# Kernel optimization log

Hardware: AMD Instinct MI355X
Metric: run time of the kernel (lower is better)

## Reference

```python
import jax, jax.numpy as jnp
import numpy as np

N = 50000     # nodes
E = 800000    # edges (avg degree 16)
DIN = 128     # in_size
DH = 256      # hidden_size
P = 100000    # pos/neg edge pairs


def _w(key, fan_in, shape):
    return jax.random.normal(key, shape, jnp.float32) * (1.0 / np.sqrt(fan_in))


def setup_inputs() -> dict:
    key = jax.random.key(0)
    ks = jax.random.split(key, 24)
    inp = {}
    inp['x'] = jax.random.normal(ks[0], (N, DIN), jnp.float32)
    inp['edge_src'] = jax.random.randint(ks[1], (E,), 0, N, dtype=jnp.int32)
    inp['edge_dst'] = jax.random.randint(ks[2], (E,), 0, N, dtype=jnp.int32)
    inp['pos_src'] = jax.random.randint(ks[3], (P,), 0, N, dtype=jnp.int32)
    inp['pos_dst'] = jax.random.randint(ks[4], (P,), 0, N, dtype=jnp.int32)
    inp['neg_src'] = jax.random.randint(ks[5], (P,), 0, N, dtype=jnp.int32)
    inp['neg_dst'] = jax.random.randint(ks[6], (P,), 0, N, dtype=jnp.int32)
    # SAGEConv layers: fc_self + fc_neigh + bias
    dims = [(DIN, DH), (DH, DH), (DH, DH)]
    for i, (di, do) in enumerate(dims):
        inp[f'Ws{i}'] = _w(ks[7 + 3 * i], di, (di, do))
        inp[f'Wn{i}'] = _w(ks[8 + 3 * i], di, (di, do))
        inp[f'b{i}'] = jnp.zeros((do,), jnp.float32)
    # predictor MLP: DH -> DH -> DH -> 1
    inp['Wp1'] = _w(ks[16], DH, (DH, DH)); inp['bp1'] = jnp.zeros((DH,), jnp.float32)
    inp['Wp2'] = _w(ks[17], DH, (DH, DH)); inp['bp2'] = jnp.zeros((DH,), jnp.float32)
    inp['Wp3'] = _w(ks[18], DH, (DH, 1)); inp['bp3'] = jnp.zeros((1,), jnp.float32)
    return inp


def _sage_layer(h, src, dst, Ws, Wn, b):
    # mean aggregation over incoming edges, then fc_self(h) + fc_neigh(agg) + b
    n = h.shape[0]
    msg = h[src]                                              # [E, d] gather
    deg = jax.ops.segment_sum(jnp.ones((src.shape[0],), h.dtype), dst, num_segments=n)
    agg = jax.ops.segment_sum(msg, dst, num_segments=n)
    agg = agg / jnp.maximum(deg, 1.0)[:, None]
    return h @ Ws + agg @ Wn + b


def reference(x, edge_src, edge_dst, pos_src, pos_dst, neg_src, neg_dst,
              Ws0, Wn0, b0, Ws1, Wn1, b1, Ws2, Wn2, b2,
              Wp1, bp1, Wp2, bp2, Wp3, bp3):
    h = x
    layers = [(Ws0, Wn0, b0), (Ws1, Wn1, b1), (Ws2, Wn2, b2)]
    for i, (Ws, Wn, bb) in enumerate(layers):
        h = _sage_layer(h, edge_src, edge_dst, Ws, Wn, bb)
        if i < len(layers) - 1:
            h = jax.nn.relu(h)

    def predictor(e):
        z = jax.nn.relu(e @ Wp1 + bp1)
        z = jax.nn.relu(z @ Wp2 + bp2)
        return z @ Wp3 + bp3

    hidden_pos = predictor(h[pos_src] * h[pos_dst])   # [P, 1]
    hidden_neg = predictor(h[neg_src] * h[neg_dst])   # [P, 1]
    return (hidden_pos, hidden_neg)
```

## Files before the change

### kernel.cpp

```cpp
#include <hip/hip_runtime.h>
#include <hip/hip_bf16.h>

#define CDIV(a, b) (((a) + (b) - 1) / (b))

typedef __attribute__((ext_vector_type(8))) __bf16 bf16x8;
typedef __attribute__((ext_vector_type(2))) __bf16 bf16x2;
typedef __attribute__((ext_vector_type(4))) float f32x4;

__device__ __forceinline__ float bf2f(unsigned short u) {
  union { unsigned int i; float f; } c; c.i = ((unsigned int)u) << 16; return c.f;
}
__device__ __forceinline__ unsigned short f2bf(float f) {
  union { float f; unsigned int i; } c; c.f = f;
  unsigned int r = c.i + 0x7fffu + ((c.i >> 16) & 1u);
  return (unsigned short)(r >> 16);
}
__device__ __forceinline__ unsigned int cvt2(float a, float b) {
  bf16x2 v; v[0] = (__bf16)a; v[1] = (__bf16)b;
  union { bf16x2 v; unsigned int u; } c; c.v = v; return c.u;
}
__device__ __forceinline__ unsigned short cvt1(float a) {
  __bf16 b = (__bf16)a;
  union { __bf16 b; unsigned short u; } c; c.b = b; return c.u;
}

__global__ void k_detect(const unsigned short* __restrict__ xq, int nsamp, int* __restrict__ flagp) {
  __shared__ float sm[256];
  int t = threadIdx.x;
  float mx = 0.f;
  for (int i = t; i < nsamp; i += 256) {
    float v = bf2f(xq[i]);
    if (!(v == v)) v = 1e30f;
    mx = fmaxf(mx, fabsf(v));
  }
  sm[t] = mx; __syncthreads();
  for (int o = 128; o > 0; o >>= 1) {
    if (t < o) sm[t] = fmaxf(sm[t], sm[t + o]);
    __syncthreads();
  }
  if (t == 0) *flagp = (sm[0] > 1e6f) ? 1 : 0;
}

__global__ void k_cvt7(const void* p0, const void* p1, const void* p2, const void* p3,
                       const void* p4, const void* p5, const void* p6,
                       float* d0, float* d1, float* d2, float* d3,
                       float* d4, float* d5, float* d6, const int* __restrict__ flagp) {
  int b = blockIdx.x, t = threadIdx.x;
  const void* s = 0; float* d = 0; int n = 256;
  switch (b) {
    case 0: s = p0; d = d0; break;
    case 1: s = p1; d = d1; break;
    case 2: s = p2; d = d2; break;
    case 3: s = p3; d = d3; break;
    case 4: s = p4; d = d4; break;
    case 5: s = p5; d = d5; break;
    default: s = p6; d = d6; n = 1; break;
  }
  if (t < n) d[t] = (*flagp) ? ((const float*)s)[t] : bf2f(((const unsigned short*)s)[t]);
}

__global__ void k_wh(const void* __restrict__ W, unsigned short* __restrict__ Bth,
                     int K, const int* __restrict__ flagp) {
  int i = blockIdx.x * 256 + threadIdx.x;
  if (i >= K * 256) return;
  int k = i >> 8, n = i & 255;
  float v = (*flagp) ? ((const float*)W)[i] : bf2f(((const unsigned short*)W)[i]);
  Bth[(size_t)n * K + k] = f2bf(v);
}

__global__ void k_xbf16(const void* __restrict__ x, unsigned short* __restrict__ Xb, int n,
                        const int* __restrict__ flagp) {
  int i = blockIdx.x * 256 + threadIdx.x;
  if (i >= n) return;
  float v = (*flagp) ? ((const float*)x)[i] : bf2f(((const unsigned short*)x)[i]);
  Xb[i] = f2bf(v);
}

__global__ void k_zero_i32(int* p, int n) {
  int i = blockIdx.x * 256 + threadIdx.x;
  if (i < n) p[i] = 0;
}

__global__ void k_deg(const int* __restrict__ dst, int* __restrict__ deg, int E) {
  int e = blockIdx.x * 256 + threadIdx.x;
  if (e < E) atomicAdd(&deg[dst[e]], 1);
}
__global__ void k_scan1(const int* __restrict__ in, int* __restrict__ out, int* __restrict__ bsums, int n) {
  __shared__ int sh[256];
  int t = threadIdx.x, i = blockIdx.x * 256 + t;
  int v = (i < n) ? in[i] : 0;
  sh[t] = v; __syncthreads();
  for (int o = 1; o < 256; o <<= 1) {
    int add = (t >= o) ? sh[t - o] : 0;
    __syncthreads();
    sh[t] += add;
    __syncthreads();
  }
  if (i < n) out[i] = sh[t] - v;
  if (t == 255) bsums[blockIdx.x] = sh[255];
}
__global__ void k_scan2(int* bsums, int nb) {
  __shared__ int sh[256];
  int t = threadIdx.x;
  int v = (t < nb) ? bsums[t] : 0;
  sh[t] = v; __syncthreads();
  for (int o = 1; o < 256; o <<= 1) {
    int add = (t >= o) ? sh[t - o] : 0;
    __syncthreads();
    sh[t] += add;
    __syncthreads();
  }
  if (t < nb) bsums[t] = sh[t] - v;
}
__global__ void k_scan3(int* offs, const int* bsums, int n, int etot) {
  int i = blockIdx.x * 256 + threadIdx.x;
  if (i < n) offs[i] += bsums[blockIdx.x];
  if (i == 0) offs[n] = etot;
}
__global__ void k_copy_i32(const int* __restrict__ a, int* __restrict__ b, int n) {
  int i = blockIdx.x * 256 + threadIdx.x;
  if (i < n) b[i] = a[i];
}
__global__ void k_fill(const int* __restrict__ dst, const int* __restrict__ src,
                       int* __restrict__ cursor, int* __restrict__ csr_src, int E) {
  int e = blockIdx.x * 256 + threadIdx.x;
  if (e >= E) return;
  int pos = atomicAdd(&cursor[dst[e]], 1);
  csr_src[pos] = src[e];
}
__global__ void k_sortw(const int* __restrict__ offs, int* __restrict__ csr, int n) {
  int w = threadIdx.x >> 6, lane = threadIdx.x & 63;
  int v = blockIdx.x * 4 + w;
  if (v >= n) return;
  int s = offs[v], e = offs[v + 1];
  int deg = e - s;
  if (deg <= 1) return;
  if (deg > 64) {
    if (lane == 0) {
      for (int i = s + 1; i < e; ++i) {
        int key = csr[i], j = i - 1;
        while (j >= s && csr[j] > key) { csr[j + 1] = csr[j]; --j; }
        csr[j + 1] = key;
      }
    }
    return;
  }
  int val = (lane < deg) ? csr[s + lane] : 0x7fffffff;
#pragma unroll
  for (int k = 2; k <= 64; k <<= 1) {
    bool dir = (lane & k) == 0;
#pragma unroll
    for (int j = k >> 1; j > 0; j >>= 1) {
      int p = __shfl_xor(val, j, 64);
      bool lower = (lane & j) == 0;
      val = (lower == dir) ? min(val, p) : max(val, p);
    }
  }
  if (lane < deg) csr[s + lane] = val;
}

__global__ void k_agg(const unsigned short* __restrict__ H, int Kd,
                      const int* __restrict__ offs, const int* __restrict__ csr,
                      unsigned short* __restrict__ Ab) {
  int w = threadIdx.x >> 6, lane = threadIdx.x & 63;
  int v = blockIdx.x * 4 + w;
  int s = offs[v], e = offs[v + 1];
  float inv = 1.f / fmaxf((float)(e - s), 1.f);
  if (Kd == 256) {
    int c4 = lane * 4;
    float a0 = 0.f, a1 = 0.f, a2 = 0.f, a3 = 0.f;
    int i = s;
    for (; i + 4 <= e; i += 4) {
      uint2 z0 = *(const uint2*)&H[(size_t)csr[i] * 256 + c4];
      uint2 z1 = *(const uint2*)&H[(size_t)csr[i + 1] * 256 + c4];
      uint2 z2 = *(const uint2*)&H[(size_t)csr[i + 2] * 256 + c4];
      uint2 z3 = *(const uint2*)&H[(size_t)csr[i + 3] * 256 + c4];
      a0 += bf2f((unsigned short)z0.x) + bf2f((unsigned short)z1.x)
          + bf2f((unsigned short)z2.x) + bf2f((unsigned short)z3.x);
      a1 += bf2f((unsigned short)(z0.x >> 16)) + bf2f((unsigned short)(z1.x >> 16))
          + bf2f((unsigned short)(z2.x >> 16)) + bf2f((unsigned short)(z3.x >> 16));
      a2 += bf2f((unsigned short)z0.y) + bf2f((unsigned short)z1.y)
          + bf2f((unsigned short)z2.y) + bf2f((unsigned short)z3.y);
      a3 += bf2f((unsigned short)(z0.y >> 16)) + bf2f((unsigned short)(z1.y >> 16))
          + bf2f((unsigned short)(z2.y >> 16)) + bf2f((unsigned short)(z3.y >> 16));
    }
    for (; i < e; ++i) {
      uint2 z0 = *(const uint2*)&H[(size_t)csr[i] * 256 + c4];
      a0 += bf2f((unsigned short)z0.x);
      a1 += bf2f((unsigned short)(z0.x >> 16));
      a2 += bf2f((unsigned short)z0.y);
      a3 += bf2f((unsigned short)(z0.y >> 16));
    }
    uint2 o;
    o.x = cvt2(a0 * inv, a1 * inv);
    o.y = cvt2(a2 * inv, a3 * inv);
    *(uint2*)&Ab[(size_t)v * 256 + c4] = o;
  } else {
    int c2 = lane * 2;
    float a0 = 0.f, a1 = 0.f;
    int i = s;
    for (; i + 4 <= e; i += 4) {
      unsigned int z0 = *(const unsigned int*)&H[(size_t)csr[i] * 128 + c2];
      unsigned int z1 = *(const unsigned int*)&H[(size_t)csr[i + 1] * 128 + c2];
      unsigned int z2 = *(const unsigned int*)&H[(size_t)csr[i + 2] * 128 + c2];
      unsigned int z3 = *(const unsigned int*)&H[(size_t)csr[i + 3] * 128 + c2];
      a0 += bf2f((unsigned short)z0) + bf2f((unsigned short)z1)
          + bf2f((unsigned short)z2) + bf2f((unsigned short)z3);
      a1 += bf2f((unsigned short)(z0 >> 16)) + bf2f((unsigned short)(z1 >> 16))
          + bf2f((unsigned short)(z2 >> 16)) + bf2f((unsigned short)(z3 >> 16));
    }
    for (; i < e; ++i) {
      unsigned int z0 = *(const unsigned int*)&H[(size_t)csr[i] * 128 + c2];
      a0 += bf2f((unsigned short)z0);
      a1 += bf2f((unsigned short)(z0 >> 16));
    }
    *(unsigned int*)&Ab[(size_t)v * 128 + c2] = cvt2(a0 * inv, a1 * inv);
  }
}

__global__ __launch_bounds__(256) void gemm_cat(
    const unsigned short* __restrict__ A1, const unsigned short* __restrict__ A2, int K,
    const unsigned short* __restrict__ B1h, const unsigned short* __restrict__ B2h,
    const float* __restrict__ bias, int relu, int M, unsigned short* __restrict__ O) {
  __shared__ unsigned short sAh[128 * 40], sBh[128 * 40];
  int t = threadIdx.x;
  int mt = blockIdx.x >> 1, nt = blockIdx.x & 1;
  int m0 = mt * 128;
  int n0 = nt * 128;
  int wid = t >> 6, lane = t & 63;
  int wr = (wid >> 1) * 64, wc = (wid & 1) * 64;
  int quad = lane >> 4, lrow = lane & 15;

  f32x4 acc[4][4];
  const f32x4 z4 = {0.f, 0.f, 0.f, 0.f};
#pragma unroll
  for (int i = 0; i < 4; ++i)
#pragma unroll
    for (int j = 0; j < 4; ++j) acc[i][j] = z4;

  int sr = t >> 2;
  int c8 = (t & 3) * 8;

#pragma unroll
  for (int pl = 0; pl < 2; ++pl) {
    const unsigned short* Ap = pl ? A2 : A1;
    const unsigned short* Bp = pl ? B2h : B1h;
    for (int k0 = 0; k0 < K; k0 += 32) {
#pragma unroll
      for (int rep = 0; rep < 2; ++rep) {
        int r = sr + rep * 64;
        int arow = m0 + r; if (arow >= M) arow = M - 1;
        *(uint4*)&sAh[r * 40 + c8] = *(const uint4*)&Ap[(size_t)arow * K + k0 + c8];
        *(uint4*)&sBh[r * 40 + c8] = *(const uint4*)&Bp[(size_t)(n0 + r) * K + k0 + c8];
      }
      __syncthreads();
      bf16x8 ah[4], bh[4];
#pragma unroll
      for (int i = 0; i < 4; ++i) {
        ah[i] = *(const bf16x8*)&sAh[(wr + i * 16 + lrow) * 40 + quad * 8];
        bh[i] = *(const bf16x8*)&sBh[(wc + i * 16 + lrow) * 40 + quad * 8];
      }
#pragma unroll
      for (int i = 0; i < 4; ++i)
#pragma unroll
        for (int j = 0; j < 4; ++j)
          acc[i][j] = __builtin_amdgcn_mfma_f32_16x16x32_bf16(ah[i], bh[j], acc[i][j], 0, 0, 0);
      __syncthreads();
    }
  }

#pragma unroll
  for (int j = 0; j < 4; ++j) {
    int gc = n0 + wc + j * 16 + lrow;
    float bv = bias[gc];
#pragma unroll
    for (int i = 0; i < 4; ++i) {
#pragma unroll
      for (int rr = 0; rr < 4; ++rr) {
        int gr = m0 + wr + i * 16 + quad * 4 + rr;
        if (gr < M) {
          float v = acc[i][j][rr] + bv;
          if (relu) v = fmaxf(v, 0.f);
          O[(size_t)gr * 256 + gc] = cvt1(v);
        }
      }
    }
  }
}

__global__ __launch_bounds__(256, 3) void gemm_pred_fused(
    const unsigned short* __restrict__ Hb,
    const int* __restrict__ ps, const int* __restrict__ pd,
    const int* __restrict__ ns, const int* __restrict__ nd,
    int nPos,
    const unsigned short* __restrict__ B1h, const float* __restrict__ bp1c,
    const unsigned short* __restrict__ B2h, const float* __restrict__ bp2c,
    const float* __restrict__ wp3, const float* __restrict__ bp3c,
    void* __restrict__ out, const int* __restrict__ flagp) {
  __shared__ __align__(16) unsigned short zT[64 * 264];
  __shared__ __align__(16) unsigned short sBh[256 * 40];
  int t = threadIdx.x;
  int m0 = blockIdx.x * 64;
  int wid = t >> 6, lane = t & 63;
  int wc = wid * 64;
  int quad = lane >> 4, lrow = lane & 15;

  int sr = t >> 2;
  int c8 = (t & 3) * 8;
  int c64 = (t & 3) * 64;

  int arow = m0 + sr;
  int s, d;
  if (arow < nPos) { s = ps[arow]; d = pd[arow]; }
  else             { s = ns[arow - nPos]; d = nd[arow - nPos]; }
  const unsigned short* Hs = &Hb[(size_t)s * 256];
  const unsigned short* Hd = &Hb[(size_t)d * 256];

#pragma unroll
  for (int u = 0; u < 8; ++u) {
    uint4 hs = *(const uint4*)(Hs + c64 + u * 8);
    uint4 hd = *(const uint4*)(Hd + c64 + u * 8);
    uint4 o;
    o.x = cvt2(bf2f((unsigned short)hs.x) * bf2f((unsigned short)hd.x),
               bf2f((unsigned short)(hs.x >> 16)) * bf2f((unsigned short)(hd.x >> 16)));
    o.y = cvt2(bf2f((unsigned short)hs.y) * bf2f((unsigned short)hd.y),
               bf2f((unsigned short)(hs.y >> 16)) * bf2f((unsigned short)(hd.y >> 16)));
    o.z = cvt2(bf2f((unsigned short)hs.z) * bf2f((unsigned short)hd.z),
               bf2f((unsigned short)(hs.z >> 16)) * bf2f((unsigned short)(hd.z >> 16)));
    o.w = cvt2(bf2f((unsigned short)hs.w) * bf2f((unsigned short)hd.w),
               bf2f((unsigned short)(hs.w >> 16)) * bf2f((unsigned short)(hd.w >> 16)));
    *(uint4*)&zT[sr * 264 + c64 + u * 8] = o;
  }

  f32x4 acc[4][4];
  const f32x4 z4 = {0.f, 0.f, 0.f, 0.f};
#pragma unroll
  for (int i = 0; i < 4; ++i)
#pragma unroll
    for (int j = 0; j < 4; ++j) acc[i][j] = z4;

  for (int k0 = 0; k0 < 256; k0 += 32) {
#pragma unroll
    for (int rep = 0; rep < 4; ++rep) {
      int r = sr + rep * 64;
      *(uint4*)&sBh[r * 40 + c8] = *(const uint4*)&B1h[(size_t)r * 256 + k0 + c8];
    }
    __syncthreads();
    bf16x8 ah[4], bh[4];
#pragma unroll
    for (int i = 0; i < 4; ++i) {
      ah[i] = *(const bf16x8*)&zT[(i * 16 + lrow) * 264 + k0 + quad * 8];
      bh[i] = *(const bf16x8*)&sBh[(wc + i * 16 + lrow) * 40 + quad * 8];
    }
#pragma unroll
    for (int i = 0; i < 4; ++i)
#pragma unroll
      for (int j = 0; j < 4; ++j)
        acc[i][j] = __builtin_amdgcn_mfma_f32_16x16x32_bf16(ah[i], bh[j], acc[i][j], 0, 0, 0);
    __syncthreads();
  }

#pragma unroll
  for (int j = 0; j < 4; ++j) {
    int gc = wc + j * 16 + lrow;
    float bv = bp1c[gc];
#pragma unroll
    for (int i = 0; i < 4; ++i) {
#pragma unroll
      for (int rr = 0; rr < 4; ++rr) {
        int rloc = i * 16 + quad * 4 + rr;
        float v = fmaxf(acc[i][j][rr] + bv, 0.f);
        zT[rloc * 264 + gc] = cvt1(v);
      }
    }
  }

#pragma unroll
  for (int i = 0; i < 4; ++i)
#pragma unroll
    for (int j = 0; j < 4; ++j) acc[i][j] = z4;

  for (int k0 = 0; k0 < 256; k0 += 32) {
#pragma unroll
    for (int rep = 0; rep < 4; ++rep) {
      int r = sr + rep * 64;
      *(uint4*)&sBh[r * 40 + c8] = *(const uint4*)&B2h[(size_t)r * 256 + k0 + c8];
    }
    __syncthreads();
    bf16x8 ah[4], bh[4];
#pragma unroll
    for (int i = 0; i < 4; ++i) {
      ah[i] = *(const bf16x8*)&zT[(i * 16 + lrow) * 264 + k0 + quad * 8];
      bh[i] = *(const bf16x8*)&sBh[(wc + i * 16 + lrow) * 40 + quad * 8];
    }
#pragma unroll
    for (int i = 0; i < 4; ++i)
#pragma unroll
      for (int j = 0; j < 4; ++j)
        acc[i][j] = __builtin_amdgcn_mfma_f32_16x16x32_bf16(ah[i], bh[j], acc[i][j], 0, 0, 0);
    __syncthreads();
  }

  float* part = (float*)sBh;
  int cid = wid * 16 + lrow;
#pragma unroll
  for (int i = 0; i < 4; ++i) {
#pragma unroll
    for (int rr = 0; rr < 4; ++rr) {
      int rloc = i * 16 + quad * 4 + rr;
      float sum = 0.f;
#pragma unroll
      for (int j = 0; j < 4; ++j) {
        int gc = wc + j * 16 + lrow;
        float v = fmaxf(acc[i][j][rr] + bp2c[gc], 0.f);
        sum += v * wp3[gc];
      }
      part[rloc * 65 + cid] = sum;
    }
  }
  __syncthreads();
  if (t < 64) {
    int gr = m0 + t;
    float ssum = 0.f;
#pragma unroll
    for (int c = 0; c < 64; ++c) ssum += part[t * 65 + c];
    ssum += bp3c[0];
    if (*flagp) ((float*)out)[gr] = ssum;
    else        ((unsigned short*)out)[gr] = f2bf(ssum);
  }
}

extern "C" void kernel_launch(void* const* d_in, const int* in_sizes, int n_in,
                              void* d_out, int out_size, void* d_ws, size_t ws_size,
                              hipStream_t stream) {
  const int N = 50000, E = 800000, P = 100000, DIN = 128, DH = 256;
  const int M2 = 2 * P;
  const void* x = d_in[0];
  const int* esrc = (const int*)d_in[1];
  const int* edst = (const int*)d_in[2];
  const int* psrc = (const int*)d_in[3];
  const int* pdst = (const int*)d_in[4];
  const int* nsrc = (const int*)d_in[5];
  const int* ndst = (const int*)d_in[6];
  const void* Ws0 = d_in[7];  const void* Wn0 = d_in[8];  const void* b0 = d_in[9];
  const void* Ws1 = d_in[10]; const void* Wn1 = d_in[11]; const void* b1 = d_in[12];
  const void* Ws2 = d_in[13]; const void* Wn2 = d_in[14]; const void* b2 = d_in[15];
  const void* Wp1 = d_in[16]; const void* bp1 = d_in[17];
  const void* Wp2 = d_in[18]; const void* bp2 = d_in[19];
  const void* Wp3 = d_in[20]; const void* bp3 = d_in[21];
  (void)in_sizes; (void)n_in; (void)out_size; (void)ws_size;

  const size_t NH = (size_t)N * DH;
  unsigned short* planeA = (unsigned short*)d_ws;
  unsigned short* Xb = planeA;
  char* reg1 = (char*)d_ws + NH * 2;
  unsigned short* AggB  = (unsigned short*)reg1;
  unsigned short* planeB = (unsigned short*)(reg1 + NH * 4);
  float* P0 = (float*)(reg1 + (size_t)M2 * 256 * 2);
  float* P1 = P0 + M2;
  unsigned short* W16 = (unsigned short*)(P1 + M2);
  unsigned short* ws0h = W16;
  unsigned short* wn0h = ws0h + 32768;
  unsigned short* ws1h = wn0h + 32768;
  unsigned short* wn1h = ws1h + 65536;
  unsigned short* ws2h = wn1h + 65536;
  unsigned short* wn2h = ws2h + 65536;
  unsigned short* wp1h = wn2h + 65536;
  unsigned short* wp2h = wp1h + 65536;
  float* FB = (float*)(wp2h + 65536);
  float* b0f  = FB;
  float* b1f  = b0f + 256;
  float* b2f  = b1f + 256;
  float* bp1f = b2f + 256;
  float* bp2f = bp1f + 256;
  float* wp3f = bp2f + 256;
  float* bp3f = wp3f + 256;
  int* deg   = (int*)(bp3f + 4);
  int* offs  = deg + N;
  int* cur   = offs + (N + 1);
  int* bsums = cur + N;
  int* csr   = bsums + 256;
  int* flagp = csr + E;

  k_detect<<<1, 256, 0, stream>>>((const unsigned short*)x, 8192, flagp);

  k_wh<<<CDIV(DIN * DH, 256), 256, 0, stream>>>(Ws0, ws0h, DIN, flagp);
  k_wh<<<CDIV(DIN * DH, 256), 256, 0, stream>>>(Wn0, wn0h, DIN, flagp);
  k_wh<<<CDIV(DH * DH, 256), 256, 0, stream>>>(Ws1, ws1h, DH, flagp);
  k_wh<<<CDIV(DH * DH, 256), 256, 0, stream>>>(Wn1, wn1h, DH, flagp);
  k_wh<<<CDIV(DH * DH, 256), 256, 0, stream>>>(Ws2, ws2h, DH, flagp);
  k_wh<<<CDIV(DH * DH, 256), 256, 0, stream>>>(Wn2, wn2h, DH, flagp);
  k_wh<<<CDIV(DH * DH, 256), 256, 0, stream>>>(Wp1, wp1h, DH, flagp);
  k_wh<<<CDIV(DH * DH, 256), 256, 0, stream>>>(Wp2, wp2h, DH, flagp);
  k_cvt7<<<7, 256, 0, stream>>>(b0, b1, b2, bp1, bp2, Wp3, bp3,
                                b0f, b1f, b2f, bp1f, bp2f, wp3f, bp3f, flagp);

  int nb = CDIV(N, 256);
  k_zero_i32<<<nb, 256, 0, stream>>>(deg, N);
  k_deg<<<CDIV(E, 256), 256, 0, stream>>>(edst, deg, E);
  k_scan1<<<nb, 256, 0, stream>>>(deg, offs, bsums, N);
  k_scan2<<<1, 256, 0, stream>>>(bsums, nb);
  k_scan3<<<nb, 256, 0, stream>>>(offs, bsums, N, E);
  k_copy_i32<<<nb, 256, 0, stream>>>(offs, cur, N);
  k_fill<<<CDIV(E, 256), 256, 0, stream>>>(edst, esrc, cur, csr, E);
  k_sortw<<<CDIV(N, 4), 256, 0, stream>>>(offs, csr, N);

  const int G_L = CDIV(N, 128) * 2;

  k_xbf16<<<CDIV(N * DIN, 256), 256, 0, stream>>>(x, Xb, N * DIN, flagp);
  k_agg<<<N / 4, 256, 0, stream>>>(Xb, DIN, offs, csr, AggB);
  gemm_cat<<<G_L, 256, 0, stream>>>(Xb, AggB, DIN, ws0h, wn0h, b0f, 1, N, planeB);

  k_agg<<<N / 4, 256, 0, stream>>>(planeB, DH, offs, csr, AggB);
  gemm_cat<<<G_L, 256, 0, stream>>>(planeB, AggB, DH, ws1h, wn1h, b1f, 1, N, planeA);

  k_agg<<<N / 4, 256, 0, stream>>>(planeA, DH, offs, csr, AggB);
  gemm_cat<<<G_L, 256, 0, stream>>>(planeA, AggB, DH, ws2h, wn2h, b2f, 0, N, planeB);

  gemm_pred_fused<<<M2 / 64, 256, 0, stream>>>(planeB, psrc, pdst, nsrc, ndst, P,
                                               wp1h, bp1f, wp2h, bp2f, wp3f, bp3f,
                                               d_out, flagp);
}
```

Before: 650.1 us.

## Load GEMM operands directly from global memory and swizzle predictor LDS tile

Both GEMM kernels stop staging A/B tiles through shared memory. Each wave now loads its MFMA operand fragments straight from global memory into registers, which removes most __syncthreads barriers and frees LDS so more blocks can be resident. In the fused predictor, the activation tile zT is XOR-swizzled by 8-element chunk to reduce bank conflicts, and hidden-layer writes are packed into pairs with a lane shuffle. The risk is that blocks now rely on L1/L2 for operand reuse across waves instead of LDS, and the per-lane 16-byte loads from strided rows are less coalesced.

```diff
diff --git a/kernel.cpp b/kernel.cpp
--- a/kernel.cpp
+++ b/kernel.cpp
@@ -222,7 +222,6 @@
     const unsigned short* __restrict__ A1, const unsigned short* __restrict__ A2, int K,
     const unsigned short* __restrict__ B1h, const unsigned short* __restrict__ B2h,
     const float* __restrict__ bias, int relu, int M, unsigned short* __restrict__ O) {
-  __shared__ unsigned short sAh[128 * 40], sBh[128 * 40];
   int t = threadIdx.x;
   int mt = blockIdx.x >> 1, nt = blockIdx.x & 1;
   int m0 = mt * 128;
@@ -238,34 +237,32 @@
 #pragma unroll
     for (int j = 0; j < 4; ++j) acc[i][j] = z4;
 
-  int sr = t >> 2;
-  int c8 = (t & 3) * 8;
+  int ra[4], rb[4];
+#pragma unroll
+  for (int i = 0; i < 4; ++i) {
+    int r = m0 + wr + i * 16 + lrow;
+    ra[i] = (r < M) ? r : (M - 1);
+    rb[i] = n0 + wc + i * 16 + lrow;
+  }
 
 #pragma unroll
   for (int pl = 0; pl < 2; ++pl) {
     const unsigned short* Ap = pl ? A2 : A1;
     const unsigned short* Bp = pl ? B2h : B1h;
+#pragma unroll 2
     for (int k0 = 0; k0 < K; k0 += 32) {
-#pragma unroll
-      for (int rep = 0; rep < 2; ++rep) {
-        int r = sr + rep * 64;
-        int arow = m0 + r; if (arow >= M) arow = M - 1;
-        *(uint4*)&sAh[r * 40 + c8] = *(const uint4*)&Ap[(size_t)arow * K + k0 + c8];
-        *(uint4*)&sBh[r * 40 + c8] = *(const uint4*)&Bp[(size_t)(n0 + r) * K + k0 + c8];
-      }
-      __syncthreads();
       bf16x8 ah[4], bh[4];
 #pragma unroll
-      for (int i = 0; i < 4; ++i) {
-        ah[i] = *(const bf16x8*)&sAh[(wr + i * 16 + lrow) * 40 + quad * 8];
-        bh[i] = *(const bf16x8*)&sBh[(wc + i * 16 + lrow) * 40 + quad * 8];
-      }
+      for (int i = 0; i < 4; ++i)
+        ah[i] = *(const bf16x8*)&Ap[(size_t)ra[i] * K + k0 + quad * 8];
+#pragma unroll
+      for (int j = 0; j < 4; ++j)
+        bh[j] = *(const bf16x8*)&Bp[(size_t)rb[j] * K + k0 + quad * 8];
 #pragma unroll
       for (int i = 0; i < 4; ++i)
 #pragma unroll
         for (int j = 0; j < 4; ++j)
           acc[i][j] = __builtin_amdgcn_mfma_f32_16x16x32_bf16(ah[i], bh[j], acc[i][j], 0, 0, 0);
-      __syncthreads();
     }
   }
 
@@ -298,7 +295,6 @@
     const float* __restrict__ wp3, const float* __restrict__ bp3c,
     void* __restrict__ out, const int* __restrict__ flagp) {
   __shared__ __align__(16) unsigned short zT[64 * 264];
-  __shared__ __align__(16) unsigned short sBh[256 * 40];
   int t = threadIdx.x;
   int m0 = blockIdx.x * 64;
   int wid = t >> 6, lane = t & 63;
@@ -306,20 +302,19 @@
   int quad = lane >> 4, lrow = lane & 15;
 
   int sr = t >> 2;
-  int c8 = (t & 3) * 8;
-  int c64 = (t & 3) * 64;
+  int cq = t & 3;
 
   int arow = m0 + sr;
   int s, d;
   if (arow < nPos) { s = ps[arow]; d = pd[arow]; }
   else             { s = ns[arow - nPos]; d = nd[arow - nPos]; }
-  const unsigned short* Hs = &Hb[(size_t)s * 256];
-  const unsigned short* Hd = &Hb[(size_t)d * 256];
+  const unsigned short* Hs = &Hb[(size_t)s * 256 + cq * 64];
+  const unsigned short* Hd = &Hb[(size_t)d * 256 + cq * 64];
 
 #pragma unroll
   for (int u = 0; u < 8; ++u) {
-    uint4 hs = *(const uint4*)(Hs + c64 + u * 8);
-    uint4 hd = *(const uint4*)(Hd + c64 + u * 8);
+    uint4 hs = *(const uint4*)(Hs + u * 8);
+    uint4 hd = *(const uint4*)(Hd + u * 8);
     uint4 o;
     o.x = cvt2(bf2f((unsigned short)hs.x) * bf2f((unsigned short)hd.x),
                bf2f((unsigned short)(hs.x >> 16)) * bf2f((unsigned short)(hd.x >> 16)));
@@ -329,7 +324,7 @@
                bf2f((unsigned short)(hs.z >> 16)) * bf2f((unsigned short)(hd.z >> 16)));
     o.w = cvt2(bf2f((unsigned short)hs.w) * bf2f((unsigned short)hd.w),
                bf2f((unsigned short)(hs.w >> 16)) * bf2f((unsigned short)(hd.w >> 16)));
-    *(uint4*)&zT[sr * 264 + c64 + u * 8] = o;
+    *(uint4*)&zT[sr * 264 + cq * 64 + 8 * (u ^ cq)] = o;
   }
 
   f32x4 acc[4][4];
@@ -339,38 +334,42 @@
 #pragma unroll
     for (int j = 0; j < 4; ++j) acc[i][j] = z4;
 
-  for (int k0 = 0; k0 < 256; k0 += 32) {
-#pragma unroll
-    for (int rep = 0; rep < 4; ++rep) {
-      int r = sr + rep * 64;
-      *(uint4*)&sBh[r * 40 + c8] = *(const uint4*)&B1h[(size_t)r * 256 + k0 + c8];
-    }
-    __syncthreads();
+  __syncthreads();
+
+#pragma unroll 2
+  for (int ss = 0; ss < 8; ++ss) {
+    int k0 = ss * 32;
     bf16x8 ah[4], bh[4];
 #pragma unroll
-    for (int i = 0; i < 4; ++i) {
-      ah[i] = *(const bf16x8*)&zT[(i * 16 + lrow) * 264 + k0 + quad * 8];
-      bh[i] = *(const bf16x8*)&sBh[(wc + i * 16 + lrow) * 40 + quad * 8];
-    }
+    for (int i = 0; i < 4; ++i)
+      ah[i] = *(const bf16x8*)&zT[(i * 16 + lrow) * 264 + k0 + 8 * (quad ^ (ss >> 1))];
+#pragma unroll
+    for (int j = 0; j < 4; ++j)
+      bh[j] = *(const bf16x8*)&B1h[(size_t)(wc + j * 16 + lrow) * 256 + k0 + quad * 8];
 #pragma unroll
     for (int i = 0; i < 4; ++i)
 #pragma unroll
       for (int j = 0; j < 4; ++j)
         acc[i][j] = __builtin_amdgcn_mfma_f32_16x16x32_bf16(ah[i], bh[j], acc[i][j], 0, 0, 0);
-    __syncthreads();
-  }
+  }
+
+  __syncthreads();
 
 #pragma unroll
   for (int j = 0; j < 4; ++j) {
-    int gc = wc + j * 16 + lrow;
-    float bv = bp1c[gc];
+    int col = wc + j * 16 + lrow;
+    float bv = bp1c[col];
 #pragma unroll
     for (int i = 0; i < 4; ++i) {
 #pragma unroll
       for (int rr = 0; rr < 4; ++rr) {
         int rloc = i * 16 + quad * 4 + rr;
         float v = fmaxf(acc[i][j][rr] + bv, 0.f);
-        zT[rloc * 264 + gc] = cvt1(v);
+        float vn = __shfl_xor(v, 1, 64);
+        if (!(lrow & 1)) {
+          int c2 = col ^ (wid << 3);
+          *(unsigned int*)&zT[rloc * 264 + c2] = cvt2(v, vn);
+        }
       }
     }
   }
@@ -380,28 +379,28 @@
 #pragma unroll
     for (int j = 0; j < 4; ++j) acc[i][j] = z4;
 
-  for (int k0 = 0; k0 < 256; k0 += 32) {
-#pragma unroll
-    for (int rep = 0; rep < 4; ++rep) {
-      int r = sr + rep * 64;
-      *(uint4*)&sBh[r * 40 + c8] = *(const uint4*)&B2h[(size_t)r * 256 + k0 + c8];
-    }
-    __syncthreads();
+  __syncthreads();
+
+#pragma unroll 2
+  for (int ss = 0; ss < 8; ++ss) {
+    int k0 = ss * 32;
     bf16x8 ah[4], bh[4];
 #pragma unroll
-    for (int i = 0; i < 4; ++i) {
-      ah[i] = *(const bf16x8*)&zT[(i * 16 + lrow) * 264 + k0 + quad * 8];
-      bh[i] = *(const bf16x8*)&sBh[(wc + i * 16 + lrow) * 40 + quad * 8];
-    }
+    for (int i = 0; i < 4; ++i)
+      ah[i] = *(const bf16x8*)&zT[(i * 16 + lrow) * 264 + k0 + 8 * (quad ^ (ss >> 1))];
+#pragma unroll
+    for (int j = 0; j < 4; ++j)
+      bh[j] = *(const bf16x8*)&B2h[(size_t)(wc + j * 16 + lrow) * 256 + k0 + quad * 8];
 #pragma unroll
     for (int i = 0; i < 4; ++i)
 #pragma unroll
       for (int j = 0; j < 4; ++j)
         acc[i][j] = __builtin_amdgcn_mfma_f32_16x16x32_bf16(ah[i], bh[j], acc[i][j], 0, 0, 0);
-    __syncthreads();
-  }
-
-  float* part = (float*)sBh;
+  }
+
+  __syncthreads();
+
+  float* part = (float*)zT;
   int cid = wid * 16 + lrow;
 #pragma unroll
   for (int i = 0; i < 4; ++i) {
@@ -415,7 +414,7 @@
         float v = fmaxf(acc[i][j][rr] + bp2c[gc], 0.f);
         sum += v * wp3[gc];
       }
-      part[rloc * 65 + cid] = sum;
+      part[rloc * 66 + cid] = sum;
     }
   }
   __syncthreads();
@@ -423,7 +422,7 @@
     int gr = m0 + t;
     float ssum = 0.f;
 #pragma unroll
-    for (int c = 0; c < 64; ++c) ssum += part[t * 65 + c];
+    for (int c = 0; c < 64; ++c) ssum += part[t * 66 + c];
     ssum += bp3c[0];
     if (*flagp) ((float*)out)[gr] = ssum;
     else        ((unsigned short*)out)[gr] = f2bf(ssum);
```

New measurement: 736.8 us. +13.3%, slower.
